# Kernel tuning notes

Measured on AMD Instinct MI355X. Metric: run time of the kernel, lower is better.

The kernel has to match this reference:

```python
import jax, jax.numpy as jnp
import numpy as np

L, B, C_IN, C_OUT, C_COND = 4096, 16, 512, 512, 512
K, RATIO, TEMPERATURE = 4, 4, 30.0
HID = C_COND // RATIO


def setup_inputs() -> dict:
    key = jax.random.key(0)
    ks = jax.random.split(key, 8)
    s_in = 1.0 / np.sqrt(C_IN)
    s_c = 1.0 / np.sqrt(C_COND)
    s_h = 1.0 / np.sqrt(HID)
    return {
        "x": jax.random.normal(ks[0], (L, B, C_IN), jnp.float32),
        "cond": jax.random.normal(ks[1], (B, C_COND), jnp.float32),
        "fc1_w": jax.random.normal(ks[2], (HID, C_COND), jnp.float32) * s_c,
        "fc1_b": jnp.zeros((HID,), jnp.float32),
        "fc2_w": jax.random.normal(ks[3], (K, HID), jnp.float32) * s_h,
        "fc2_b": jnp.zeros((K,), jnp.float32),
        "weight": jax.random.normal(ks[4], (K, C_OUT, C_IN), jnp.float32) * s_in,
        "bias": jax.random.normal(ks[5], (K, C_OUT), jnp.float32) * s_in,
    }


def reference(x, cond, fc1_w, fc1_b, fc2_w, fc2_b, weight, bias):
    # attention over K kernel banks, conditioned on style vector
    h = jax.nn.relu(cond @ fc1_w.T + fc1_b)          # (B, HID)
    logits = h @ fc2_w.T + fc2_b                     # (B, K)
    att = jax.nn.softmax(logits / TEMPERATURE, axis=-1)
    # per-sample aggregated 1x1-conv weight/bias (the grouped conv, groups=B)
    w_agg = jnp.einsum("bk,koi->boi", att, weight)   # (B, C_OUT, C_IN)
    b_agg = att @ bias                               # (B, C_OUT)
    # per-sample matmul over tokens: (L,B,C_in) x (B,C_out,C_in) -> (L,B,C_out)
    out = jnp.einsum("lbi,boi->lbo", x, w_agg) + b_agg[None, :, :]
    return out
```

## Files before the change

kernel.cpp:

```cpp
#include <hip/hip_runtime.h>
#include <hip/hip_bf16.h>

typedef __bf16 bfx8 __attribute__((ext_vector_type(8)));
typedef float f32x4 __attribute__((ext_vector_type(4)));
typedef unsigned short u16x8 __attribute__((ext_vector_type(8)));
typedef unsigned short u16x4 __attribute__((ext_vector_type(4)));

__device__ __forceinline__ unsigned short f2bf(float f) {
    unsigned int u = __builtin_bit_cast(unsigned int, f);
    u += 0x7fffu + ((u >> 16) & 1u);
    return (unsigned short)(u >> 16);
}

__device__ __forceinline__ int swz_idx(int row, int chunk) {
    const int p = row >> 1;
    const int q = (((row & 1) << 2) | chunk) ^ (p & 7);
    return p * 64 + q * 8;
}

__global__ __launch_bounds__(1024) void att_kernel(
    const float* __restrict__ cond, const float* __restrict__ fc1w,
    const float* __restrict__ fc1b, const float* __restrict__ fc2w,
    const float* __restrict__ fc2b, const float* __restrict__ bias,
    float* __restrict__ att_out, float* __restrict__ bagg_out)
{
    __shared__ float h[128];
    __shared__ float att_s[4];
    const int b    = blockIdx.x;
    const int tid  = threadIdx.x;
    const int lane = tid & 63;
    const int wv   = tid >> 6;

    for (int j = wv; j < 128; j += 16) {
        const float* c = cond + b * 512 + lane * 8;
        const float* w = fc1w + j * 512 + lane * 8;
        const float4 c0 = *(const float4*)c, c1 = *(const float4*)(c + 4);
        const float4 w0 = *(const float4*)w, w1 = *(const float4*)(w + 4);
        float s = c0.x * w0.x + c0.y * w0.y + c0.z * w0.z + c0.w * w0.w
                + c1.x * w1.x + c1.y * w1.y + c1.z * w1.z + c1.w * w1.w;
        #pragma unroll
        for (int off = 32; off; off >>= 1) s += __shfl_down(s, off);
        if (lane == 0) h[j] = fmaxf(s + fc1b[j], 0.0f);
    }
    __syncthreads();

    if (wv < 4) {
        const int k = wv;
        float s = h[lane] * fc2w[k * 128 + lane] + h[lane + 64] * fc2w[k * 128 + lane + 64];
        #pragma unroll
        for (int off = 32; off; off >>= 1) s += __shfl_down(s, off);
        if (lane == 0) att_s[k] = (s + fc2b[k]) * (1.0f / 30.0f);
    }
    __syncthreads();

    if (tid == 0) {
        float l0 = att_s[0], l1 = att_s[1], l2 = att_s[2], l3 = att_s[3];
        float m = fmaxf(fmaxf(l0, l1), fmaxf(l2, l3));
        float e0 = expf(l0 - m), e1 = expf(l1 - m), e2 = expf(l2 - m), e3 = expf(l3 - m);
        float inv = 1.0f / (e0 + e1 + e2 + e3);
        att_s[0] = e0 * inv; att_s[1] = e1 * inv; att_s[2] = e2 * inv; att_s[3] = e3 * inv;
        att_out[b * 4 + 0] = att_s[0]; att_out[b * 4 + 1] = att_s[1];
        att_out[b * 4 + 2] = att_s[2]; att_out[b * 4 + 3] = att_s[3];
    }
    __syncthreads();

    if (tid < 512) {
        bagg_out[b * 512 + tid] = att_s[0] * bias[tid] + att_s[1] * bias[512 + tid]
                                + att_s[2] * bias[1024 + tid] + att_s[3] * bias[1536 + tid];
    }
}

__global__ __launch_bounds__(256) void wagg_kernel(
    const float* __restrict__ weight, const float* __restrict__ att,
    unsigned short* __restrict__ wagg)
{
    __shared__ float a_s[64];
    if (threadIdx.x < 64) a_s[threadIdx.x] = att[threadIdx.x];
    __syncthreads();
    const int p = (blockIdx.x * 256 + threadIdx.x) * 4;
    const float4 w0 = *(const float4*)(weight + p);
    const float4 w1 = *(const float4*)(weight + 262144 + p);
    const float4 w2 = *(const float4*)(weight + 524288 + p);
    const float4 w3 = *(const float4*)(weight + 786432 + p);
    #pragma unroll
    for (int b = 0; b < 16; ++b) {
        const float a0 = a_s[4 * b], a1 = a_s[4 * b + 1], a2 = a_s[4 * b + 2], a3 = a_s[4 * b + 3];
        u16x4 r;
        r[0] = f2bf(a0 * w0.x + a1 * w1.x + a2 * w2.x + a3 * w3.x);
        r[1] = f2bf(a0 * w0.y + a1 * w1.y + a2 * w2.y + a3 * w3.y);
        r[2] = f2bf(a0 * w0.z + a1 * w1.z + a2 * w2.z + a3 * w3.z);
        r[3] = f2bf(a0 * w0.w + a1 * w1.w + a2 * w2.w + a3 * w3.w);
        *(u16x4*)(wagg + (size_t)b * 262144 + p) = r;
    }
}

__global__ __launch_bounds__(512, 2) void gemm_kernel(
    const float* __restrict__ x, const unsigned short* __restrict__ wagg,
    const float* __restrict__ bagg, float* __restrict__ out)
{
    __shared__ unsigned short As[2][128 * 32];
    __shared__ unsigned short Bs[2][512 * 32];
    __shared__ float bsh[512];

    const int tid = threadIdx.x;
    const int bid = blockIdx.x;
    const int b  = bid >> 5;
    const int l0 = (bid & 31) * 128;

    const int lane = tid & 63;
    const int wid  = tid >> 6;
    const int wm   = wid >> 2;
    const int wn   = wid & 3;
    const int fr   = lane & 15;
    const int fq   = lane >> 4;

    const unsigned short* wb = wagg + (size_t)b * (512 * 512);

    bsh[tid] = bagg[b * 512 + tid];

    f32x4 acc[4][8];
    #pragma unroll
    for (int i = 0; i < 4; ++i)
        #pragma unroll
        for (int j = 0; j < 8; ++j) acc[i][j] = f32x4{0.f, 0.f, 0.f, 0.f};

    const int ea   = tid * 8;
    const int arow = ea >> 5;
    const int achk = (ea & 31) >> 3;
    const int aswz = swz_idx(arow, achk);
    const float* xsrc = x + ((size_t)(l0 + arow) * 16 + b) * 512 + (ea & 31);

    int bofs[4];
    #pragma unroll
    for (int it = 0; it < 4; ++it) {
        const int s = it * 512 + tid;
        const int p = s >> 3, q = s & 7;
        const int v = q ^ (p & 7);
        const int row = (p << 1) | (v >> 2);
        const int cch = v & 3;
        bofs[it] = row * 512 + cch * 8;
    }

    int aidx[4], bidx[8];
    #pragma unroll
    for (int mf = 0; mf < 4; ++mf) aidx[mf] = swz_idx(wm * 64 + mf * 16 + fr, fq);
    #pragma unroll
    for (int nf = 0; nf < 8; ++nf) bidx[nf] = swz_idx(wn * 128 + nf * 16 + fr, fq);

    {
        const float4 v0 = *(const float4*)(xsrc);
        const float4 v1 = *(const float4*)(xsrc + 4);
        u16x8 pk;
        pk[0] = f2bf(v0.x); pk[1] = f2bf(v0.y); pk[2] = f2bf(v0.z); pk[3] = f2bf(v0.w);
        pk[4] = f2bf(v1.x); pk[5] = f2bf(v1.y); pk[6] = f2bf(v1.z); pk[7] = f2bf(v1.w);
        *(u16x8*)&As[0][aswz] = pk;
        #pragma unroll
        for (int it = 0; it < 4; ++it) {
            char* dst = (char*)&Bs[0][0] + it * 8192 + tid * 16;
            __builtin_amdgcn_global_load_lds(
                (const __attribute__((address_space(1))) void*)(wb + bofs[it]),
                (__attribute__((address_space(3))) void*)dst, 16, 0, 0);
        }
    }
    __syncthreads();

    int cur = 0;
    for (int kt = 0; kt < 16; ++kt) {
        const int nxt = cur ^ 1;
        float4 v0, v1;
        if (kt < 15) {
            const int k0n = (kt + 1) * 32;
            #pragma unroll
            for (int it = 0; it < 4; ++it) {
                char* dst = (char*)&Bs[nxt][0] + it * 8192 + tid * 16;
                __builtin_amdgcn_global_load_lds(
                    (const __attribute__((address_space(1))) void*)(wb + bofs[it] + k0n),
                    (__attribute__((address_space(3))) void*)dst, 16, 0, 0);
            }
            v0 = *(const float4*)(xsrc + k0n);
            v1 = *(const float4*)(xsrc + k0n + 4);
        }
        bfx8 af[4], bfr[8];
        #pragma unroll
        for (int mf = 0; mf < 4; ++mf)
            af[mf] = *reinterpret_cast<const bfx8*>(&As[cur][aidx[mf]]);
        #pragma unroll
        for (int nf = 0; nf < 8; ++nf)
            bfr[nf] = *reinterpret_cast<const bfx8*>(&Bs[cur][bidx[nf]]);
        #pragma unroll
        for (int mf = 0; mf < 4; ++mf)
            #pragma unroll
            for (int nf = 0; nf < 8; ++nf)
                acc[mf][nf] = __builtin_amdgcn_mfma_f32_16x16x32_bf16(af[mf], bfr[nf], acc[mf][nf], 0, 0, 0);
        if (kt < 15) {
            u16x8 pk;
            pk[0] = f2bf(v0.x); pk[1] = f2bf(v0.y); pk[2] = f2bf(v0.z); pk[3] = f2bf(v0.w);
            pk[4] = f2bf(v1.x); pk[5] = f2bf(v1.y); pk[6] = f2bf(v1.z); pk[7] = f2bf(v1.w);
            *(u16x8*)&As[nxt][aswz] = pk;
            __syncthreads();
            cur = nxt;
        }
    }

    #pragma unroll
    for (int mf = 0; mf < 4; ++mf) {
        #pragma unroll
        for (int nf = 0; nf < 8; ++nf) {
            const int o = wn * 128 + nf * 16 + fr;
            const float bb = bsh[o];
            const int lrow = l0 + wm * 64 + mf * 16 + fq * 4;
            float* op = out + ((size_t)lrow * 16 + b) * 512 + o;
            const f32x4 a = acc[mf][nf];
            op[0]        = a[0] + bb;
            op[8192]     = a[1] + bb;
            op[2 * 8192] = a[2] + bb;
            op[3 * 8192] = a[3] + bb;
        }
    }
}

extern "C" void kernel_launch(void* const* d_in, const int* in_sizes, int n_in,
                              void* d_out, int out_size, void* d_ws, size_t ws_size,
                              hipStream_t stream) {
    const float* x      = (const float*)d_in[0];
    const float* cond   = (const float*)d_in[1];
    const float* fc1w   = (const float*)d_in[2];
    const float* fc1b   = (const float*)d_in[3];
    const float* fc2w   = (const float*)d_in[4];
    const float* fc2b   = (const float*)d_in[5];
    const float* weight = (const float*)d_in[6];
    const float* bias   = (const float*)d_in[7];
    float* out = (float*)d_out;

    char* ws = (char*)d_ws;
    float* att_ws  = (float*)ws;
    float* bagg_ws = (float*)(ws + 1024);
    unsigned short* wagg_ws = (unsigned short*)(ws + 65536);

    att_kernel<<<16, 1024, 0, stream>>>(cond, fc1w, fc1b, fc2w, fc2b, bias, att_ws, bagg_ws);
    wagg_kernel<<<256, 256, 0, stream>>>(weight, att_ws, wagg_ws);
    gemm_kernel<<<512, 512, 0, stream>>>(x, wagg_ws, bagg_ws, out);
}
```

Measured before the change: 90.12 us.

## Split GEMM output N into 128-wide tiles with 256-thread blocks

The GEMM kernel moves from one block covering all 512 output channels of a 128-row tile (512 threads, 8 waves) to four blocks each covering 128 output channels (256 threads, 4 waves), for 2048 blocks instead of 512. Per-block shared memory and accumulators shrink, so more blocks can be resident and the grid fills the CUs better. The cost is that every x tile is now read and converted to bf16 four times instead of once, which adds global traffic and conversion work. Scheduling barriers are added around the x prefetch loads.

```diff
diff --git a/kernel.cpp b/kernel.cpp
--- a/kernel.cpp
+++ b/kernel.cpp
@@ -94,46 +94,51 @@
     }
 }
 
-__global__ __launch_bounds__(512, 2) void gemm_kernel(
+__global__ __launch_bounds__(256, 3) void gemm_kernel(
     const float* __restrict__ x, const unsigned short* __restrict__ wagg,
     const float* __restrict__ bagg, float* __restrict__ out)
 {
     __shared__ unsigned short As[2][128 * 32];
-    __shared__ unsigned short Bs[2][512 * 32];
-    __shared__ float bsh[512];
+    __shared__ unsigned short Bs[2][128 * 32];
+    __shared__ float bsh[128];
 
     const int tid = threadIdx.x;
     const int bid = blockIdx.x;
-    const int b  = bid >> 5;
-    const int l0 = (bid & 31) * 128;
+    const int b  = bid >> 7;
+    const int lt = (bid >> 2) & 31;
+    const int nt = bid & 3;
+    const int l0 = lt * 128;
+    const int n0 = nt * 128;
 
     const int lane = tid & 63;
     const int wid  = tid >> 6;
-    const int wm   = wid >> 2;
-    const int wn   = wid & 3;
+    const int wm   = wid >> 1;
+    const int wn   = wid & 1;
     const int fr   = lane & 15;
     const int fq   = lane >> 4;
 
-    const unsigned short* wb = wagg + (size_t)b * (512 * 512);
-
-    bsh[tid] = bagg[b * 512 + tid];
-
-    f32x4 acc[4][8];
+    const unsigned short* wb = wagg + (size_t)b * (512 * 512) + (size_t)n0 * 512;
+
+    if (tid < 128) bsh[tid] = bagg[b * 512 + n0 + tid];
+
+    f32x4 acc[4][4];
     #pragma unroll
     for (int i = 0; i < 4; ++i)
         #pragma unroll
-        for (int j = 0; j < 8; ++j) acc[i][j] = f32x4{0.f, 0.f, 0.f, 0.f};
-
-    const int ea   = tid * 8;
-    const int arow = ea >> 5;
-    const int achk = (ea & 31) >> 3;
-    const int aswz = swz_idx(arow, achk);
-    const float* xsrc = x + ((size_t)(l0 + arow) * 16 + b) * 512 + (ea & 31);
-
-    int bofs[4];
-    #pragma unroll
-    for (int it = 0; it < 4; ++it) {
-        const int s = it * 512 + tid;
+        for (int j = 0; j < 4; ++j) acc[i][j] = f32x4{0.f, 0.f, 0.f, 0.f};
+
+    const int ar0 = tid >> 2;
+    const int ar1 = ar0 + 64;
+    const int ac  = (tid & 3) * 8;
+    const int aswz0 = swz_idx(ar0, tid & 3);
+    const int aswz1 = swz_idx(ar1, tid & 3);
+    const float* xs0 = x + ((size_t)(l0 + ar0) * 16 + b) * 512 + ac;
+    const float* xs1 = x + ((size_t)(l0 + ar1) * 16 + b) * 512 + ac;
+
+    int bofs[2];
+    #pragma unroll
+    for (int it = 0; it < 2; ++it) {
+        const int s = tid + it * 256;
         const int p = s >> 3, q = s & 7;
         const int v = q ^ (p & 7);
         const int row = (p << 1) | (v >> 2);
@@ -141,22 +146,27 @@
         bofs[it] = row * 512 + cch * 8;
     }
 
-    int aidx[4], bidx[8];
+    int aidx[4], bidx[4];
     #pragma unroll
     for (int mf = 0; mf < 4; ++mf) aidx[mf] = swz_idx(wm * 64 + mf * 16 + fr, fq);
     #pragma unroll
-    for (int nf = 0; nf < 8; ++nf) bidx[nf] = swz_idx(wn * 128 + nf * 16 + fr, fq);
+    for (int nf = 0; nf < 4; ++nf) bidx[nf] = swz_idx(wn * 64 + nf * 16 + fr, fq);
 
     {
-        const float4 v0 = *(const float4*)(xsrc);
-        const float4 v1 = *(const float4*)(xsrc + 4);
+        const float4 v0 = *(const float4*)(xs0);
+        const float4 v1 = *(const float4*)(xs0 + 4);
+        const float4 v2 = *(const float4*)(xs1);
+        const float4 v3 = *(const float4*)(xs1 + 4);
         u16x8 pk;
         pk[0] = f2bf(v0.x); pk[1] = f2bf(v0.y); pk[2] = f2bf(v0.z); pk[3] = f2bf(v0.w);
         pk[4] = f2bf(v1.x); pk[5] = f2bf(v1.y); pk[6] = f2bf(v1.z); pk[7] = f2bf(v1.w);
-        *(u16x8*)&As[0][aswz] = pk;
-        #pragma unroll
-        for (int it = 0; it < 4; ++it) {
-            char* dst = (char*)&Bs[0][0] + it * 8192 + tid * 16;
+        *(u16x8*)&As[0][aswz0] = pk;
+        pk[0] = f2bf(v2.x); pk[1] = f2bf(v2.y); pk[2] = f2bf(v2.z); pk[3] = f2bf(v2.w);
+        pk[4] = f2bf(v3.x); pk[5] = f2bf(v3.y); pk[6] = f2bf(v3.z); pk[7] = f2bf(v3.w);
+        *(u16x8*)&As[0][aswz1] = pk;
+        #pragma unroll
+        for (int it = 0; it < 2; ++it) {
+            char* dst = (char*)&Bs[0][0] + (tid + it * 256) * 16;
             __builtin_amdgcn_global_load_lds(
                 (const __attribute__((address_space(1))) void*)(wb + bofs[it]),
                 (__attribute__((address_space(3))) void*)dst, 16, 0, 0);
@@ -167,36 +177,43 @@
     int cur = 0;
     for (int kt = 0; kt < 16; ++kt) {
         const int nxt = cur ^ 1;
-        float4 v0, v1;
+        float4 v0, v1, v2, v3;
         if (kt < 15) {
             const int k0n = (kt + 1) * 32;
             #pragma unroll
-            for (int it = 0; it < 4; ++it) {
-                char* dst = (char*)&Bs[nxt][0] + it * 8192 + tid * 16;
+            for (int it = 0; it < 2; ++it) {
+                char* dst = (char*)&Bs[nxt][0] + (tid + it * 256) * 16;
                 __builtin_amdgcn_global_load_lds(
                     (const __attribute__((address_space(1))) void*)(wb + bofs[it] + k0n),
                     (__attribute__((address_space(3))) void*)dst, 16, 0, 0);
             }
-            v0 = *(const float4*)(xsrc + k0n);
-            v1 = *(const float4*)(xsrc + k0n + 4);
-        }
-        bfx8 af[4], bfr[8];
+            __builtin_amdgcn_sched_barrier(0);
+            v0 = *(const float4*)(xs0 + k0n);
+            v1 = *(const float4*)(xs0 + k0n + 4);
+            v2 = *(const float4*)(xs1 + k0n);
+            v3 = *(const float4*)(xs1 + k0n + 4);
+            __builtin_amdgcn_sched_barrier(0);
+        }
+        bfx8 af[4], bfr[4];
         #pragma unroll
         for (int mf = 0; mf < 4; ++mf)
             af[mf] = *reinterpret_cast<const bfx8*>(&As[cur][aidx[mf]]);
         #pragma unroll
-        for (int nf = 0; nf < 8; ++nf)
+        for (int nf = 0; nf < 4; ++nf)
             bfr[nf] = *reinterpret_cast<const bfx8*>(&Bs[cur][bidx[nf]]);
         #pragma unroll
         for (int mf = 0; mf < 4; ++mf)
             #pragma unroll
-            for (int nf = 0; nf < 8; ++nf)
+            for (int nf = 0; nf < 4; ++nf)
                 acc[mf][nf] = __builtin_amdgcn_mfma_f32_16x16x32_bf16(af[mf], bfr[nf], acc[mf][nf], 0, 0, 0);
         if (kt < 15) {
             u16x8 pk;
             pk[0] = f2bf(v0.x); pk[1] = f2bf(v0.y); pk[2] = f2bf(v0.z); pk[3] = f2bf(v0.w);
             pk[4] = f2bf(v1.x); pk[5] = f2bf(v1.y); pk[6] = f2bf(v1.z); pk[7] = f2bf(v1.w);
-            *(u16x8*)&As[nxt][aswz] = pk;
+            *(u16x8*)&As[nxt][aswz0] = pk;
+            pk[0] = f2bf(v2.x); pk[1] = f2bf(v2.y); pk[2] = f2bf(v2.z); pk[3] = f2bf(v2.w);
+            pk[4] = f2bf(v3.x); pk[5] = f2bf(v3.y); pk[6] = f2bf(v3.z); pk[7] = f2bf(v3.w);
+            *(u16x8*)&As[nxt][aswz1] = pk;
             __syncthreads();
             cur = nxt;
         }
@@ -205,11 +222,11 @@
     #pragma unroll
     for (int mf = 0; mf < 4; ++mf) {
         #pragma unroll
-        for (int nf = 0; nf < 8; ++nf) {
-            const int o = wn * 128 + nf * 16 + fr;
-            const float bb = bsh[o];
+        for (int nf = 0; nf < 4; ++nf) {
+            const int on = wn * 64 + nf * 16 + fr;
+            const float bb = bsh[on];
             const int lrow = l0 + wm * 64 + mf * 16 + fq * 4;
-            float* op = out + ((size_t)lrow * 16 + b) * 512 + o;
+            float* op = out + ((size_t)lrow * 16 + b) * 512 + n0 + on;
             const f32x4 a = acc[mf][nf];
             op[0]        = a[0] + bb;
             op[8192]     = a[1] + bb;
@@ -239,5 +256,5 @@
 
     att_kernel<<<16, 1024, 0, stream>>>(cond, fc1w, fc1b, fc2w, fc2b, bias, att_ws, bagg_ws);
     wagg_kernel<<<256, 256, 0, stream>>>(weight, att_ws, wagg_ws);
-    gemm_kernel<<<512, 512, 0, stream>>>(x, wagg_ws, bagg_ws, out);
-}
+    gemm_kernel<<<2048, 256, 0, stream>>>(x, wagg_ws, bagg_ws, out);
+}
```

Measured after the change: 125.6 us. +39.4%, slower.

## Keep full weight tile resident in LDS and stream x directly into registers

Applied to the files above, without the earlier changes.

The GEMM is restructured so each workgroup loads a 128x512 bf16 slice of the aggregated weight into LDS once, with an XOR swizzle. Activations are read straight from global memory into registers with a one-step prefetch and converted to bf16 in-register, which removes the A-tile LDS staging and the per-k-step barriers. The tile shape changes to 512 tokens by 128 outputs, and workgroup ordering is remapped so neighbouring workgroups share x or weight. In exchange, each x element is read by four workgroups, LDS use grows to 128KB, and register pressure rises, which may reduce occupancy.

```diff
diff --git a/kernel.cpp b/kernel.cpp
--- a/kernel.cpp
+++ b/kernel.cpp
@@ -3,6 +3,7 @@
 
 typedef __bf16 bfx8 __attribute__((ext_vector_type(8)));
 typedef float f32x4 __attribute__((ext_vector_type(4)));
+typedef float f32x8v __attribute__((ext_vector_type(8)));
 typedef unsigned short u16x8 __attribute__((ext_vector_type(8)));
 typedef unsigned short u16x4 __attribute__((ext_vector_type(4)));
 
@@ -12,10 +13,9 @@
     return (unsigned short)(u >> 16);
 }
 
-__device__ __forceinline__ int swz_idx(int row, int chunk) {
-    const int p = row >> 1;
-    const int q = (((row & 1) << 2) | chunk) ^ (p & 7);
-    return p * 64 + q * 8;
+__device__ __forceinline__ bfx8 cvt8(float4 a, float4 b) {
+    f32x8v v = {a.x, a.y, a.z, a.w, b.x, b.y, b.z, b.w};
+    return __builtin_convertvector(v, bfx8);
 }
 
 __global__ __launch_bounds__(1024) void att_kernel(
@@ -98,118 +98,98 @@
     const float* __restrict__ x, const unsigned short* __restrict__ wagg,
     const float* __restrict__ bagg, float* __restrict__ out)
 {
-    __shared__ unsigned short As[2][128 * 32];
-    __shared__ unsigned short Bs[2][512 * 32];
-    __shared__ float bsh[512];
+    __shared__ unsigned short Ws[128 * 512];
 
     const int tid = threadIdx.x;
-    const int bid = blockIdx.x;
-    const int b  = bid >> 5;
-    const int l0 = (bid & 31) * 128;
+    const int wgid = (blockIdx.x & 7) * 64 + (blockIdx.x >> 3);
+    const int fam  = wgid >> 3;
+    const int lg   = wgid & 7;
+    const int b    = fam >> 2;
+    const int nt   = fam & 3;
+    const int l0   = lg * 512;
+    const int n0   = nt * 128;
 
     const int lane = tid & 63;
     const int wid  = tid >> 6;
-    const int wm   = wid >> 2;
-    const int wn   = wid & 3;
+    const int wm   = wid >> 1;
+    const int wn   = wid & 1;
     const int fr   = lane & 15;
     const int fq   = lane >> 4;
 
-    const unsigned short* wb = wagg + (size_t)b * (512 * 512);
-
-    bsh[tid] = bagg[b * 512 + tid];
-
-    f32x4 acc[4][8];
-    #pragma unroll
-    for (int i = 0; i < 4; ++i)
-        #pragma unroll
-        for (int j = 0; j < 8; ++j) acc[i][j] = f32x4{0.f, 0.f, 0.f, 0.f};
-
-    const int ea   = tid * 8;
-    const int arow = ea >> 5;
-    const int achk = (ea & 31) >> 3;
-    const int aswz = swz_idx(arow, achk);
-    const float* xsrc = x + ((size_t)(l0 + arow) * 16 + b) * 512 + (ea & 31);
-
-    int bofs[4];
-    #pragma unroll
-    for (int it = 0; it < 4; ++it) {
-        const int s = it * 512 + tid;
-        const int p = s >> 3, q = s & 7;
-        const int v = q ^ (p & 7);
-        const int row = (p << 1) | (v >> 2);
-        const int cch = v & 3;
-        bofs[it] = row * 512 + cch * 8;
-    }
-
-    int aidx[4], bidx[8];
-    #pragma unroll
-    for (int mf = 0; mf < 4; ++mf) aidx[mf] = swz_idx(wm * 64 + mf * 16 + fr, fq);
-    #pragma unroll
-    for (int nf = 0; nf < 8; ++nf) bidx[nf] = swz_idx(wn * 128 + nf * 16 + fr, fq);
-
-    {
-        const float4 v0 = *(const float4*)(xsrc);
-        const float4 v1 = *(const float4*)(xsrc + 4);
-        u16x8 pk;
-        pk[0] = f2bf(v0.x); pk[1] = f2bf(v0.y); pk[2] = f2bf(v0.z); pk[3] = f2bf(v0.w);
-        pk[4] = f2bf(v1.x); pk[5] = f2bf(v1.y); pk[6] = f2bf(v1.z); pk[7] = f2bf(v1.w);
-        *(u16x8*)&As[0][aswz] = pk;
-        #pragma unroll
-        for (int it = 0; it < 4; ++it) {
-            char* dst = (char*)&Bs[0][0] + it * 8192 + tid * 16;
-            __builtin_amdgcn_global_load_lds(
-                (const __attribute__((address_space(1))) void*)(wb + bofs[it]),
-                (__attribute__((address_space(3))) void*)dst, 16, 0, 0);
-        }
-    }
-    __syncthreads();
-
-    int cur = 0;
+    const unsigned short* wb = wagg + (size_t)b * 262144 + (size_t)n0 * 512;
+
+    #pragma unroll
+    for (int it = 0; it < 16; ++it) {
+        const int s   = it * 512 + tid;
+        const int row = s >> 6;
+        const int cd  = s & 63;
+        const int csrc = (cd & ~7) | ((cd & 7) ^ (row & 7));
+        char* dst = (char*)Ws + s * 16;
+        __builtin_amdgcn_global_load_lds(
+            (const __attribute__((address_space(1))) void*)(wb + row * 512 + csrc * 8),
+            (__attribute__((address_space(3))) void*)dst, 16, 0, 0);
+    }
+
+    const float* xbase = x + ((size_t)(l0 + wm * 128 + fr) * 16 + b) * 512 + fq * 8;
+
+    int bbase[4];
+    #pragma unroll
+    for (int nf = 0; nf < 4; ++nf) bbase[nf] = (wn * 64 + nf * 16 + fr) * 512;
+    const int r7 = fr & 7;
+
+    f32x4 acc[8][4];
+    #pragma unroll
+    for (int i = 0; i < 8; ++i)
+        #pragma unroll
+        for (int j = 0; j < 4; ++j) acc[i][j] = f32x4{0.f, 0.f, 0.f, 0.f};
+
+    float4 xp[16];
+    #pragma unroll
+    for (int mf = 0; mf < 8; ++mf) {
+        const float* p = xbase + (size_t)mf * 16 * 8192;
+        xp[2 * mf]     = *(const float4*)(p);
+        xp[2 * mf + 1] = *(const float4*)(p + 4);
+    }
+
+    __syncthreads();
+
     for (int kt = 0; kt < 16; ++kt) {
-        const int nxt = cur ^ 1;
-        float4 v0, v1;
+        const int koff = ((kt >> 1) * 8 + (((kt & 1) * 4 + fq) ^ r7)) * 8;
+        bfx8 bfr[4];
+        #pragma unroll
+        for (int nf = 0; nf < 4; ++nf)
+            bfr[nf] = *reinterpret_cast<const bfx8*>(&Ws[bbase[nf] + koff]);
+        float4 xn[16];
         if (kt < 15) {
-            const int k0n = (kt + 1) * 32;
+            const int ko = (kt + 1) * 32;
             #pragma unroll
-            for (int it = 0; it < 4; ++it) {
-                char* dst = (char*)&Bs[nxt][0] + it * 8192 + tid * 16;
-                __builtin_amdgcn_global_load_lds(
-                    (const __attribute__((address_space(1))) void*)(wb + bofs[it] + k0n),
-                    (__attribute__((address_space(3))) void*)dst, 16, 0, 0);
+            for (int mf = 0; mf < 8; ++mf) {
+                const float* p = xbase + (size_t)mf * 16 * 8192 + ko;
+                xn[2 * mf]     = *(const float4*)(p);
+                xn[2 * mf + 1] = *(const float4*)(p + 4);
             }
-            v0 = *(const float4*)(xsrc + k0n);
-            v1 = *(const float4*)(xsrc + k0n + 4);
-        }
-        bfx8 af[4], bfr[8];
-        #pragma unroll
-        for (int mf = 0; mf < 4; ++mf)
-            af[mf] = *reinterpret_cast<const bfx8*>(&As[cur][aidx[mf]]);
-        #pragma unroll
-        for (int nf = 0; nf < 8; ++nf)
-            bfr[nf] = *reinterpret_cast<const bfx8*>(&Bs[cur][bidx[nf]]);
-        #pragma unroll
-        for (int mf = 0; mf < 4; ++mf)
+        }
+        #pragma unroll
+        for (int mf = 0; mf < 8; ++mf) {
+            const bfx8 afr = cvt8(xp[2 * mf], xp[2 * mf + 1]);
             #pragma unroll
-            for (int nf = 0; nf < 8; ++nf)
-                acc[mf][nf] = __builtin_amdgcn_mfma_f32_16x16x32_bf16(af[mf], bfr[nf], acc[mf][nf], 0, 0, 0);
+            for (int nf = 0; nf < 4; ++nf)
+                acc[mf][nf] = __builtin_amdgcn_mfma_f32_16x16x32_bf16(afr, bfr[nf], acc[mf][nf], 0, 0, 0);
+        }
         if (kt < 15) {
-            u16x8 pk;
-            pk[0] = f2bf(v0.x); pk[1] = f2bf(v0.y); pk[2] = f2bf(v0.z); pk[3] = f2bf(v0.w);
-            pk[4] = f2bf(v1.x); pk[5] = f2bf(v1.y); pk[6] = f2bf(v1.z); pk[7] = f2bf(v1.w);
-            *(u16x8*)&As[nxt][aswz] = pk;
-            __syncthreads();
-            cur = nxt;
-        }
-    }
-
-    #pragma unroll
-    for (int mf = 0; mf < 4; ++mf) {
-        #pragma unroll
-        for (int nf = 0; nf < 8; ++nf) {
-            const int o = wn * 128 + nf * 16 + fr;
-            const float bb = bsh[o];
-            const int lrow = l0 + wm * 64 + mf * 16 + fq * 4;
-            float* op = out + ((size_t)lrow * 16 + b) * 512 + o;
+            #pragma unroll
+            for (int j = 0; j < 16; ++j) xp[j] = xn[j];
+        }
+    }
+
+    #pragma unroll
+    for (int nf = 0; nf < 4; ++nf) {
+        const int on = wn * 64 + nf * 16 + fr;
+        const float bb = bagg[b * 512 + n0 + on];
+        #pragma unroll
+        for (int mf = 0; mf < 8; ++mf) {
+            const int lrow = l0 + wm * 128 + mf * 16 + fq * 4;
+            float* op = out + ((size_t)lrow * 16 + b) * 512 + n0 + on;
             const f32x4 a = acc[mf][nf];
             op[0]        = a[0] + bb;
             op[8192]     = a[1] + bb;
```

After: 175.9 us. 95.2% more time.
